# Kernel optimization log

Measured on AMD Instinct MI355X. Metric: run time of the kernel, lower is better.

Reference implementation:

```python
import jax, jax.numpy as jnp
import numpy as np

B, L, H, NH, P = 4, 1024, 1024, 16, 2048
HD = H // NH


def setup_inputs() -> dict:
    key = jax.random.key(0)
    ks = jax.random.split(key, 6)
    x = jax.random.normal(ks[0], (B, L, H), dtype=jnp.float32)
    # torch.nn.Linear weights are [out, in]
    Wqkv = jax.random.normal(ks[1], (3 * H, H), dtype=jnp.float32) * 0.02
    bqkv = jnp.zeros((3 * H,), dtype=jnp.float32)
    Wo = jax.random.normal(ks[2], (H, H), dtype=jnp.float32) * 0.02
    bo = jnp.zeros((H,), dtype=jnp.float32)
    Er = jax.random.normal(ks[3], (NH, P, HD), dtype=jnp.float32)
    # causal mask: True where attention is disallowed (masked_fill semantics)
    mask = jnp.triu(jnp.ones((L, L), dtype=bool), k=1)
    return {"x": x, "mask": mask, "Wqkv": Wqkv, "bqkv": bqkv,
            "Wo": Wo, "bo": bo, "Er": Er}


def reference(x, mask, Wqkv, bqkv, Wo, bo, Er):
    b, l, d = x.shape
    nh, p, hd = Er.shape
    qkv = x @ Wqkv.T + bqkv                      # [b, l, 3d]
    q, k, v = jnp.split(qkv, 3, axis=-1)
    q = q.reshape(b, l, nh, hd).transpose(0, 2, 1, 3)   # [b, nh, l, hd]
    k = k.reshape(b, l, nh, hd).transpose(0, 2, 1, 3)
    v = v.reshape(b, l, nh, hd).transpose(0, 2, 1, 3)

    scores = jnp.einsum('bnlh,bnkh->bnlk', q, k) / jnp.sqrt(
        jnp.asarray(hd, dtype=x.dtype))

    # relative positions (j - i), torch negative-index wraparound -> mod p
    pos = jnp.arange(l)
    rel = (pos[None, :] - pos[:, None]) % p      # [l, l] in [0, p)
    # Equivalent to einsum('bnlh,rnlkh->bnlk', q, Er[:, rel][None]) but
    # computed as q @ Er^T over all positions then gathered (same math,
    # avoids materializing the [nh, l, l, hd] tensor).
    QEr_full = jnp.einsum('bnlh,nph->bnlp', q, Er)       # [b, nh, l, p]
    i_idx = pos[:, None]                          # broadcasts with rel
    QEr = QEr_full[:, :, i_idx, rel]              # [b, nh, l, l]

    a = scores + QEr
    a = jnp.where(mask, -jnp.inf, a)
    a = jax.nn.softmax(a, axis=-1)                # dropout: eval mode (identity)

    out = jnp.einsum('bnlk,bnkh->bnlh', a, v)     # [b, nh, l, hd]
    out = out.transpose(0, 2, 1, 3).reshape(b, l, d)
    return out @ Wo.T + bo
```

## Files before the change

kernel.cpp:

```cpp
#include <hip/hip_runtime.h>

typedef unsigned short u16;
typedef __bf16 bf16x8 __attribute__((ext_vector_type(8)));
typedef unsigned short u16x8 __attribute__((ext_vector_type(8)));
typedef float f32x4 __attribute__((ext_vector_type(4)));

#define MFMA16(a, b, c) __builtin_amdgcn_mfma_f32_16x16x32_bf16((a), (b), (c), 0, 0, 0)

#define WAVE_LDS_FENCE() do { \
  asm volatile("s_waitcnt lgkmcnt(0)" ::: "memory"); \
  __builtin_amdgcn_sched_barrier(0); \
} while (0)

#define PHASE_BARRIER() do { \
  asm volatile("s_waitcnt vmcnt(0)" ::: "memory"); \
  __builtin_amdgcn_sched_barrier(0); \
  __builtin_amdgcn_s_barrier(); \
} while (0)

#define GLDS(gp, lp) __builtin_amdgcn_global_load_lds( \
    (const __attribute__((address_space(1))) unsigned int*)(gp), \
    (__attribute__((address_space(3))) unsigned int*)(lp), 16, 0, 0)

__device__ __forceinline__ u16 f2b(float f) {
  unsigned u = __float_as_uint(f);
  u += 0x7fffu + ((u >> 16) & 1u);
  return (u16)(u >> 16);
}
__device__ __forceinline__ float b2f(u16 h) {
  return __uint_as_float(((unsigned)h) << 16);
}

__global__ void cvt_all(const float* __restrict__ x, u16* __restrict__ xb,
                        const float* __restrict__ w1, u16* __restrict__ w1b,
                        const float* __restrict__ w2, u16* __restrict__ w2b) {
  int i = blockIdx.x * blockDim.x + threadIdx.x;
  const float* s; u16* d; int off;
  if (i < 1048576)      { s = x;  d = xb;  off = i; }
  else if (i < 1835008) { s = w1; d = w1b; off = i - 1048576; }
  else                  { s = w2; d = w2b; off = i - 1835008; }
  float4 v = *(const float4*)(s + (size_t)off * 4);
  *(ushort4*)(d + (size_t)off * 4) = make_ushort4(f2b(v.x), f2b(v.y), f2b(v.z), f2b(v.w));
}

__global__ void build_F(const float* __restrict__ Er, u16* __restrict__ Fb) {
  int i = blockIdx.x * blockDim.x + threadIdx.x;
  int base = i * 4;
  int d = base & 63;
  int m = (base >> 6) & 1023;
  int n = base >> 16;
  int sm = (2048 - m) & 2047;
  float4 v = *(const float4*)(Er + ((size_t)(n * 2048 + sm) * 64 + d));
  *(ushort4*)(Fb + (size_t)base) = make_ushort4(f2b(v.x), f2b(v.y), f2b(v.z), f2b(v.w));
}

__global__ __launch_bounds__(256) void transpose_v(const u16* __restrict__ V, u16* __restrict__ Vt) {
  __shared__ u16 T[4096];
  const int bn = blockIdx.x, i0 = blockIdx.y * 64;
  const int t = threadIdx.x;
#pragma unroll
  for (int s = 0; s < 2; ++s) {
    int ch = t + 256 * s;
    int i = ch >> 3, c = ch & 7;
    u16x8 v = *(const u16x8*)&V[(size_t)((bn << 10) + i0 + i) * 64 + c * 8];
#pragma unroll
    for (int e = 0; e < 8; ++e) {
      int d = c * 8 + e;
      T[d * 64 + ((((i >> 3) ^ (d & 7) ^ ((d >> 3) & 7)) & 7) << 3) + (i & 7)] = v[e];
    }
  }
  __syncthreads();
#pragma unroll
  for (int s = 0; s < 2; ++s) {
    int ch = t + 256 * s;
    int d = ch >> 3, cc = ch & 7;
    u16x8 o = *(const u16x8*)&T[d * 64 + (((cc ^ (d & 7) ^ ((d >> 3) & 7)) & 7) << 3)];
    *(u16x8*)&Vt[(size_t)((bn << 6) + d) * 1024 + i0 + cc * 8] = o;
  }
}

__global__ __launch_bounds__(256) void gemm_qkv(const u16* __restrict__ A, const u16* __restrict__ Bw,
                                                const float* __restrict__ bias,
                                                u16* __restrict__ Qo, u16* __restrict__ Ko,
                                                u16* __restrict__ Vo) {
  __shared__ u16 As[2][4][128][8];
  __shared__ u16 Bs[2][4][128][8];
  const int m0 = blockIdx.y * 128, n0 = blockIdx.x * 128;
  const int t = threadIdx.x, lane = t & 63, w = t >> 6;
  const int wr = w >> 1, wc = w & 1;
  const int l16 = lane & 15, lg = lane >> 4;
  f32x4 acc[4][4] = {};
  const int c0 = t, r0 = c0 & 127, g0 = c0 >> 7;
  const int c1 = t + 256, r1 = c1 & 127, g1 = c1 >> 7;

#define STAGE(buf, k0) do { \
    GLDS(&A[(size_t)(m0 + r0) * 1024 + (k0) + g0 * 8], &As[buf][g0][r0][0]); \
    GLDS(&A[(size_t)(m0 + r1) * 1024 + (k0) + g1 * 8], &As[buf][g1][r1][0]); \
    GLDS(&Bw[(size_t)(n0 + r0) * 1024 + (k0) + g0 * 8], &Bs[buf][g0][r0][0]); \
    GLDS(&Bw[(size_t)(n0 + r1) * 1024 + (k0) + g1 * 8], &Bs[buf][g1][r1][0]); \
  } while (0)

  STAGE(0, 0);
  PHASE_BARRIER();

#pragma unroll 2
  for (int kt = 0; kt < 32; ++kt) {
    const int buf = kt & 1;
    if (kt < 31) STAGE(buf ^ 1, (kt + 1) * 32);
    __builtin_amdgcn_sched_barrier(0);
    bf16x8 af[4], bfr[4];
#pragma unroll
    for (int m = 0; m < 4; ++m) af[m] = *(const bf16x8*)&As[buf][lg][wr * 64 + m * 16 + l16][0];
#pragma unroll
    for (int n = 0; n < 4; ++n) bfr[n] = *(const bf16x8*)&Bs[buf][lg][wc * 64 + n * 16 + l16][0];
#pragma unroll
    for (int m = 0; m < 4; ++m)
#pragma unroll
      for (int n = 0; n < 4; ++n) acc[m][n] = MFMA16(af[m], bfr[n], acc[m][n]);
    PHASE_BARRIER();
  }
#undef STAGE

#pragma unroll
  for (int n = 0; n < 4; ++n) {
    int col = n0 + wc * 64 + n * 16 + l16;
    float bq = bias[col];
    int which = col >> 10;
    int h = col & 1023;
    int head = h >> 6, d = h & 63;
    u16* dst = which == 0 ? Qo : (which == 1 ? Ko : Vo);
    float scale = which == 1 ? 0.125f : 1.0f;
#pragma unroll
    for (int m = 0; m < 4; ++m) {
#pragma unroll
      for (int r = 0; r < 4; ++r) {
        int row = m0 + wr * 64 + m * 16 + lg * 4 + r;
        int b = row >> 10, ii = row & 1023;
        float v = (acc[m][n][r] + bq) * scale;
        dst[(size_t)(((b * 16 + head) << 10) + ii) * 64 + d] = f2b(v);
      }
    }
  }
}

__global__ __launch_bounds__(256) void gemm_out(const u16* __restrict__ A, const u16* __restrict__ Bw,
                                                const float* __restrict__ bias, float* __restrict__ Co) {
  __shared__ u16 As[2][4][128][8];
  __shared__ u16 Bs[2][4][128][8];
  const int m0 = blockIdx.y * 128, n0 = blockIdx.x * 128;
  const int t = threadIdx.x, lane = t & 63, w = t >> 6;
  const int wr = w >> 1, wc = w & 1;
  const int l16 = lane & 15, lg = lane >> 4;
  f32x4 acc[4][4] = {};
  const int c0 = t, r0 = c0 & 127, g0 = c0 >> 7;
  const int c1 = t + 256, r1 = c1 & 127, g1 = c1 >> 7;

#define STAGE(buf, k0) do { \
    GLDS(&A[(size_t)(m0 + r0) * 1024 + (k0) + g0 * 8], &As[buf][g0][r0][0]); \
    GLDS(&A[(size_t)(m0 + r1) * 1024 + (k0) + g1 * 8], &As[buf][g1][r1][0]); \
    GLDS(&Bw[(size_t)(n0 + r0) * 1024 + (k0) + g0 * 8], &Bs[buf][g0][r0][0]); \
    GLDS(&Bw[(size_t)(n0 + r1) * 1024 + (k0) + g1 * 8], &Bs[buf][g1][r1][0]); \
  } while (0)

  STAGE(0, 0);
  PHASE_BARRIER();

#pragma unroll 2
  for (int kt = 0; kt < 32; ++kt) {
    const int buf = kt & 1;
    if (kt < 31) STAGE(buf ^ 1, (kt + 1) * 32);
    __builtin_amdgcn_sched_barrier(0);
    bf16x8 af[4], bfr[4];
#pragma unroll
    for (int m = 0; m < 4; ++m) af[m] = *(const bf16x8*)&As[buf][lg][wr * 64 + m * 16 + l16][0];
#pragma unroll
    for (int n = 0; n < 4; ++n) bfr[n] = *(const bf16x8*)&Bs[buf][lg][wc * 64 + n * 16 + l16][0];
#pragma unroll
    for (int m = 0; m < 4; ++m)
#pragma unroll
      for (int n = 0; n < 4; ++n) acc[m][n] = MFMA16(af[m], bfr[n], acc[m][n]);
    PHASE_BARRIER();
  }
#undef STAGE

#pragma unroll
  for (int n = 0; n < 4; ++n) {
    int col = n0 + wc * 64 + n * 16 + l16;
    float bq = bias[col];
#pragma unroll
    for (int m = 0; m < 4; ++m) {
#pragma unroll
      for (int r = 0; r < 4; ++r) {
        int row = m0 + wr * 64 + m * 16 + lg * 4 + r;
        Co[(size_t)row * 1024 + col] = acc[m][n][r] + bq;
      }
    }
  }
}

__global__ __launch_bounds__(256) void attn_kernel(const u16* __restrict__ Qg, const u16* __restrict__ Kg,
                                                   const u16* __restrict__ Vtg, const u16* __restrict__ Fg,
                                                   u16* __restrict__ AO) {
  __shared__ u16 Kl[4096];
  __shared__ u16 Vl[4096];
  __shared__ u16 Fl[8192];
  __shared__ u16 Bnd[4][16][84];
  __shared__ u16 Pl[4][1024];

  const int bn = blockIdx.x;
  const int b = bn >> 4, n = bn & 15;
  const int qt = 15 - (int)blockIdx.y;
  const int i0 = qt * 64;
  const int t = threadIdx.x, lane = t & 63, w = t >> 6;
  const int l16 = lane & 15, lg = lane >> 4;

  const int rr0 = t >> 3, cc0 = t & 7;
  const int rr1 = (t + 256) >> 3, cc1 = t & 7;
  const int rr2 = (t + 512) >> 3, cc2 = t & 7;
  const int rr3 = (t + 768) >> 3, cc3 = t & 7;

  bf16x8 qf[2];
  {
    const u16* qp = &Qg[(size_t)((bn << 10) + i0 + (w << 4) + l16) * 64 + lg * 8];
    qf[0] = *(const bf16x8*)qp;
    qf[1] = *(const bf16x8*)(qp + 32);
  }

  float mrun[4], lsum[4];
  f32x4 ao[4] = {};
#pragma unroll
  for (int r = 0; r < 4; ++r) { mrun[r] = -3.0e38f; lsum[r] = 0.0f; }

  u16x8 rk0, rk1, rv0, rv1, rf0, rf1, rf2, rf3;

#define LOAD_STAGE(jt_) do { \
    int j0_ = (jt_) * 64, mb_ = i0 - j0_ - 63; \
    rk0 = *(const u16x8*)&Kg[(size_t)((bn << 10) + j0_ + rr0) * 64 + cc0 * 8]; \
    rk1 = *(const u16x8*)&Kg[(size_t)((bn << 10) + j0_ + rr1) * 64 + cc1 * 8]; \
    rv0 = *(const u16x8*)&Vtg[(size_t)((bn << 6) + rr0) * 1024 + j0_ + cc0 * 8]; \
    rv1 = *(const u16x8*)&Vtg[(size_t)((bn << 6) + rr1) * 1024 + j0_ + cc1 * 8]; \
    int m0_ = mb_ + rr0; m0_ = m0_ < 0 ? 0 : (m0_ > 1023 ? 1023 : m0_); \
    int m1_ = mb_ + rr1; m1_ = m1_ < 0 ? 0 : (m1_ > 1023 ? 1023 : m1_); \
    int m2_ = mb_ + rr2; m2_ = m2_ < 0 ? 0 : (m2_ > 1023 ? 1023 : m2_); \
    int m3_ = mb_ + rr3; m3_ = m3_ < 0 ? 0 : (m3_ > 1023 ? 1023 : m3_); \
    rf0 = *(const u16x8*)&Fg[(size_t)((n << 10) + m0_) * 64 + cc0 * 8]; \
    rf1 = *(const u16x8*)&Fg[(size_t)((n << 10) + m1_) * 64 + cc1 * 8]; \
    rf2 = *(const u16x8*)&Fg[(size_t)((n << 10) + m2_) * 64 + cc2 * 8]; \
    rf3 = *(const u16x8*)&Fg[(size_t)((n << 10) + m3_) * 64 + cc3 * 8]; \
  } while (0)

  LOAD_STAGE(0);

  for (int jt = 0; jt <= qt; ++jt) {
    const bool diag = (jt == qt);

    *(u16x8*)&Kl[rr0 * 64 + (((cc0 ^ (rr0 & 7)) & 7) << 3)] = rk0;
    *(u16x8*)&Kl[rr1 * 64 + (((cc1 ^ (rr1 & 7)) & 7) << 3)] = rk1;
    *(u16x8*)&Vl[rr0 * 64 + (((cc0 ^ (rr0 & 7)) & 7) << 3)] = rv0;
    *(u16x8*)&Vl[rr1 * 64 + (((cc1 ^ (rr1 & 7)) & 7) << 3)] = rv1;
    *(u16x8*)&Fl[rr0 * 64 + (((cc0 ^ (rr0 & 7)) & 7) << 3)] = rf0;
    *(u16x8*)&Fl[rr1 * 64 + (((cc1 ^ (rr1 & 7)) & 7) << 3)] = rf1;
    *(u16x8*)&Fl[rr2 * 64 + (((cc2 ^ (rr2 & 7)) & 7) << 3)] = rf2;
    *(u16x8*)&Fl[rr3 * 64 + (((cc3 ^ (rr3 & 7)) & 7) << 3)] = rf3;
    __syncthreads();

    if (jt < qt) LOAD_STAGE(jt + 1);

    f32x4 sc[4] = {};
#pragma unroll
    for (int kk = 0; kk < 2; ++kk)
#pragma unroll
      for (int nn = 0; nn < 4; ++nn) {
        int jr = nn * 16 + l16;
        bf16x8 kb = *(const bf16x8*)&Kl[jr * 64 + ((((lg + 4 * kk) ^ (jr & 7)) & 7) << 3)];
        sc[nn] = MFMA16(qf[kk], kb, sc[nn]);
      }
    f32x4 bb[5] = {};
#pragma unroll
    for (int kk = 0; kk < 2; ++kk)
#pragma unroll
      for (int ct = 0; ct < 5; ++ct) {
        int trow = (w << 4) + ct * 16 + l16;
        bf16x8 fb = *(const bf16x8*)&Fl[trow * 64 + ((((lg + 4 * kk) ^ (trow & 7)) & 7) << 3)];
        bb[ct] = MFMA16(qf[kk], fb, bb[ct]);
      }
#pragma unroll
    for (int ct = 0; ct < 5; ++ct)
#pragma unroll
      for (int r = 0; r < 4; ++r)
        Bnd[w][lg * 4 + r][ct * 16 + l16] = f2b(bb[ct][r]);
    WAVE_LDS_FENCE();

    const unsigned* bw = (const unsigned*)&Bnd[w][0][0];
    float pv[4][4];
#pragma unroll
    for (int r = 0; r < 4; ++r) {
      int il = lg * 4 + r;
      int c0 = il - l16 + 63;
      int u0 = il * 84 + c0;
      int sh = (u0 & 1) << 4;
      float stmp[4];
      float mx = -3.0e38f;
#pragma unroll
      for (int nn = 0; nn < 4; ++nn) {
        unsigned dv = bw[(u0 >> 1) - 8 * nn];
        float s = sc[nn][r] + b2f((u16)((dv >> sh) & 0xffffu));
        if (diag && (c0 - 16 * nn + (w << 4) < 63)) s = -1.0e30f;
        stmp[nn] = s;
        mx = fmaxf(mx, s);
      }
#pragma unroll
      for (int off = 1; off < 16; off <<= 1) mx = fmaxf(mx, __shfl_xor(mx, off));
      float mnew = fmaxf(mrun[r], mx);
      float scl = __expf(mrun[r] - mnew);
      float rs = 0.0f;
#pragma unroll
      for (int nn = 0; nn < 4; ++nn) {
        pv[nn][r] = __expf(stmp[nn] - mnew);
        rs += pv[nn][r];
      }
      lsum[r] = lsum[r] * scl + rs;
      mrun[r] = mnew;
#pragma unroll
      for (int nd = 0; nd < 4; ++nd) ao[nd][r] *= scl;
    }

#pragma unroll
    for (int nn = 0; nn < 4; ++nn)
#pragma unroll
      for (int r = 0; r < 4; ++r) {
        int i = lg * 4 + r, j = nn * 16 + l16;
        Pl[w][i * 64 + ((((j >> 3) ^ (i & 7)) & 7) << 3) + (j & 7)] = f2b(pv[nn][r]);
      }
    WAVE_LDS_FENCE();
#pragma unroll
    for (int kk = 0; kk < 2; ++kk) {
      bf16x8 pa = *(const bf16x8*)&Pl[w][l16 * 64 + ((((lg + 4 * kk) ^ (l16 & 7)) & 7) << 3)];
#pragma unroll
      for (int nd = 0; nd < 4; ++nd) {
        int dr = nd * 16 + l16;
        bf16x8 vb = *(const bf16x8*)&Vl[dr * 64 + ((((lg + 4 * kk) ^ (dr & 7)) & 7) << 3)];
        ao[nd] = MFMA16(pa, vb, ao[nd]);
      }
    }
    __syncthreads();
  }

#pragma unroll
  for (int r = 0; r < 4; ++r)
#pragma unroll
    for (int off = 1; off < 16; off <<= 1) lsum[r] += __shfl_xor(lsum[r], off);

#pragma unroll
  for (int nd = 0; nd < 4; ++nd)
#pragma unroll
    for (int r = 0; r < 4; ++r) {
      int i = i0 + (w << 4) + lg * 4 + r;
      int d = nd * 16 + l16;
      float v = ao[nd][r] / lsum[r];
      AO[(size_t)((b << 10) + i) * 1024 + n * 64 + d] = f2b(v);
    }
#undef LOAD_STAGE
}

extern "C" void kernel_launch(void* const* d_in, const int* in_sizes, int n_in,
                              void* d_out, int out_size, void* d_ws, size_t ws_size,
                              hipStream_t stream) {
  (void)in_sizes; (void)n_in; (void)out_size; (void)ws_size;
  const float* x    = (const float*)d_in[0];
  const float* Wqkv = (const float*)d_in[2];
  const float* bqkv = (const float*)d_in[3];
  const float* Wo   = (const float*)d_in[4];
  const float* bo   = (const float*)d_in[5];
  const float* Er   = (const float*)d_in[6];
  float* out = (float*)d_out;

  char* p = (char*)d_ws;
  u16* xb    = (u16*)p; p += (size_t)4096 * 1024 * 2;
  u16* wqkvb = (u16*)p; p += (size_t)3072 * 1024 * 2;
  u16* wob   = (u16*)p; p += (size_t)1024 * 1024 * 2;
  u16* Fb    = (u16*)p; p += (size_t)16 * 1024 * 64 * 2;
  u16* Qb    = (u16*)p; p += (size_t)64 * 1024 * 64 * 2;
  u16* Kb    = (u16*)p; p += (size_t)64 * 1024 * 64 * 2;
  u16* Vb    = (u16*)p; p += (size_t)64 * 1024 * 64 * 2;
  u16* Vtb   = (u16*)p; p += (size_t)64 * 1024 * 64 * 2;
  u16* AO    = (u16*)p; p += (size_t)4096 * 1024 * 2;

  cvt_all<<<8192, 256, 0, stream>>>(x, xb, Wqkv, wqkvb, Wo, wob);
  build_F<<<1024, 256, 0, stream>>>(Er, Fb);
  gemm_qkv<<<dim3(24, 32), 256, 0, stream>>>(xb, wqkvb, bqkv, Qb, Kb, Vb);
  transpose_v<<<dim3(64, 16), 256, 0, stream>>>(Vb, Vtb);
  attn_kernel<<<dim3(64, 16), 256, 0, stream>>>(Qb, Kb, Vtb, Fb, AO);
  gemm_out<<<dim3(8, 32), 256, 0, stream>>>(AO, wob, bo, out);
}
```

Baseline: 166.2 us.

## Triple-buffer GEMM pipelines, remap tiles per XCD, and reuse Er band rows in attention

Both GEMMs move from double-buffered LDS staging with a full vmcnt(0) wait to a three-stage ring that waits on vmcnt(4), so one prefetch stays in flight behind each compute step. Block indices are remapped so consecutive tiles on the same XCD share A/B rows, aiming at better L2 reuse. In attention, the relative-position Er band is kept in a two-half ring in LDS, so each step loads only 64 new rows instead of 128. The band gather is rewritten into a compact per-wave layout read as one u16x4 vector. s_setprio is raised around the MFMA sections. The changes add LDS use and index arithmetic, and depend on correct wait counts and ring indexing.

Result: faster. 153.0 us (-7.9%).

```diff
diff --git a/kernel.cpp b/kernel.cpp
--- a/kernel.cpp
+++ b/kernel.cpp
@@ -3,6 +3,7 @@
 typedef unsigned short u16;
 typedef __bf16 bf16x8 __attribute__((ext_vector_type(8)));
 typedef unsigned short u16x8 __attribute__((ext_vector_type(8)));
+typedef unsigned short u16x4 __attribute__((ext_vector_type(4)));
 typedef float f32x4 __attribute__((ext_vector_type(4)));
 
 #define MFMA16(a, b, c) __builtin_amdgcn_mfma_f32_16x16x32_bf16((a), (b), (c), 0, 0, 0)
@@ -12,10 +13,11 @@
   __builtin_amdgcn_sched_barrier(0); \
 } while (0)
 
-#define PHASE_BARRIER() do { \
-  asm volatile("s_waitcnt vmcnt(0)" ::: "memory"); \
+#define PIPE_WAIT(N) do { \
+  asm volatile("s_waitcnt vmcnt(" #N ")" ::: "memory"); \
   __builtin_amdgcn_sched_barrier(0); \
   __builtin_amdgcn_s_barrier(); \
+  __builtin_amdgcn_sched_barrier(0); \
 } while (0)
 
 #define GLDS(gp, lp) __builtin_amdgcn_global_load_lds( \
@@ -83,31 +85,38 @@
                                                 const float* __restrict__ bias,
                                                 u16* __restrict__ Qo, u16* __restrict__ Ko,
                                                 u16* __restrict__ Vo) {
-  __shared__ u16 As[2][4][128][8];
-  __shared__ u16 Bs[2][4][128][8];
-  const int m0 = blockIdx.y * 128, n0 = blockIdx.x * 128;
+  __shared__ u16 As[3][4][128][8];
+  __shared__ u16 Bs[3][4][128][8];
+  const int orig = blockIdx.y * 24 + blockIdx.x;
+  const int xcd = orig & 7, q = orig >> 3;
+  const int mt = ((xcd >> 1) << 3) + q / 12;
+  const int nt = (xcd & 1) * 12 + q % 12;
+  const int m0 = mt * 128, n0 = nt * 128;
   const int t = threadIdx.x, lane = t & 63, w = t >> 6;
   const int wr = w >> 1, wc = w & 1;
   const int l16 = lane & 15, lg = lane >> 4;
   f32x4 acc[4][4] = {};
-  const int c0 = t, r0 = c0 & 127, g0 = c0 >> 7;
-  const int c1 = t + 256, r1 = c1 & 127, g1 = c1 >> 7;
+  const int r0 = t & 127, g0 = t >> 7;
+  const int g1 = g0 + 2;
 
 #define STAGE(buf, k0) do { \
     GLDS(&A[(size_t)(m0 + r0) * 1024 + (k0) + g0 * 8], &As[buf][g0][r0][0]); \
-    GLDS(&A[(size_t)(m0 + r1) * 1024 + (k0) + g1 * 8], &As[buf][g1][r1][0]); \
+    GLDS(&A[(size_t)(m0 + r0) * 1024 + (k0) + g1 * 8], &As[buf][g1][r0][0]); \
     GLDS(&Bw[(size_t)(n0 + r0) * 1024 + (k0) + g0 * 8], &Bs[buf][g0][r0][0]); \
-    GLDS(&Bw[(size_t)(n0 + r1) * 1024 + (k0) + g1 * 8], &Bs[buf][g1][r1][0]); \
+    GLDS(&Bw[(size_t)(n0 + r0) * 1024 + (k0) + g1 * 8], &Bs[buf][g1][r0][0]); \
   } while (0)
 
   STAGE(0, 0);
-  PHASE_BARRIER();
-
-#pragma unroll 2
+  STAGE(1, 32);
+
+  int buf = 0;
   for (int kt = 0; kt < 32; ++kt) {
-    const int buf = kt & 1;
-    if (kt < 31) STAGE(buf ^ 1, (kt + 1) * 32);
-    __builtin_amdgcn_sched_barrier(0);
+    if (kt < 31) PIPE_WAIT(4); else PIPE_WAIT(0);
+    if (kt < 30) {
+      int nb = buf + 2; if (nb >= 3) nb -= 3;
+      STAGE(nb, (kt + 2) * 32);
+      __builtin_amdgcn_sched_barrier(0);
+    }
     bf16x8 af[4], bfr[4];
 #pragma unroll
     for (int m = 0; m < 4; ++m) af[m] = *(const bf16x8*)&As[buf][lg][wr * 64 + m * 16 + l16][0];
@@ -117,7 +126,7 @@
     for (int m = 0; m < 4; ++m)
 #pragma unroll
       for (int n = 0; n < 4; ++n) acc[m][n] = MFMA16(af[m], bfr[n], acc[m][n]);
-    PHASE_BARRIER();
+    if (++buf == 3) buf = 0;
   }
 #undef STAGE
 
@@ -145,31 +154,38 @@
 
 __global__ __launch_bounds__(256) void gemm_out(const u16* __restrict__ A, const u16* __restrict__ Bw,
                                                 const float* __restrict__ bias, float* __restrict__ Co) {
-  __shared__ u16 As[2][4][128][8];
-  __shared__ u16 Bs[2][4][128][8];
-  const int m0 = blockIdx.y * 128, n0 = blockIdx.x * 128;
+  __shared__ u16 As[3][4][128][8];
+  __shared__ u16 Bs[3][4][128][8];
+  const int orig = blockIdx.y * 8 + blockIdx.x;
+  const int xcd = orig & 7, q = orig >> 3;
+  const int mt = (xcd << 2) + (q >> 3);
+  const int nt = q & 7;
+  const int m0 = mt * 128, n0 = nt * 128;
   const int t = threadIdx.x, lane = t & 63, w = t >> 6;
   const int wr = w >> 1, wc = w & 1;
   const int l16 = lane & 15, lg = lane >> 4;
   f32x4 acc[4][4] = {};
-  const int c0 = t, r0 = c0 & 127, g0 = c0 >> 7;
-  const int c1 = t + 256, r1 = c1 & 127, g1 = c1 >> 7;
+  const int r0 = t & 127, g0 = t >> 7;
+  const int g1 = g0 + 2;
 
 #define STAGE(buf, k0) do { \
     GLDS(&A[(size_t)(m0 + r0) * 1024 + (k0) + g0 * 8], &As[buf][g0][r0][0]); \
-    GLDS(&A[(size_t)(m0 + r1) * 1024 + (k0) + g1 * 8], &As[buf][g1][r1][0]); \
+    GLDS(&A[(size_t)(m0 + r0) * 1024 + (k0) + g1 * 8], &As[buf][g1][r0][0]); \
     GLDS(&Bw[(size_t)(n0 + r0) * 1024 + (k0) + g0 * 8], &Bs[buf][g0][r0][0]); \
-    GLDS(&Bw[(size_t)(n0 + r1) * 1024 + (k0) + g1 * 8], &Bs[buf][g1][r1][0]); \
+    GLDS(&Bw[(size_t)(n0 + r0) * 1024 + (k0) + g1 * 8], &Bs[buf][g1][r0][0]); \
   } while (0)
 
   STAGE(0, 0);
-  PHASE_BARRIER();
-
-#pragma unroll 2
+  STAGE(1, 32);
+
+  int buf = 0;
   for (int kt = 0; kt < 32; ++kt) {
-    const int buf = kt & 1;
-    if (kt < 31) STAGE(buf ^ 1, (kt + 1) * 32);
-    __builtin_amdgcn_sched_barrier(0);
+    if (kt < 31) PIPE_WAIT(4); else PIPE_WAIT(0);
+    if (kt < 30) {
+      int nb = buf + 2; if (nb >= 3) nb -= 3;
+      STAGE(nb, (kt + 2) * 32);
+      __builtin_amdgcn_sched_barrier(0);
+    }
     bf16x8 af[4], bfr[4];
 #pragma unroll
     for (int m = 0; m < 4; ++m) af[m] = *(const bf16x8*)&As[buf][lg][wr * 64 + m * 16 + l16][0];
@@ -179,7 +195,7 @@
     for (int m = 0; m < 4; ++m)
 #pragma unroll
       for (int n = 0; n < 4; ++n) acc[m][n] = MFMA16(af[m], bfr[n], acc[m][n]);
-    PHASE_BARRIER();
+    if (++buf == 3) buf = 0;
   }
 #undef STAGE
 
@@ -204,7 +220,7 @@
   __shared__ u16 Kl[4096];
   __shared__ u16 Vl[4096];
   __shared__ u16 Fl[8192];
-  __shared__ u16 Bnd[4][16][84];
+  __shared__ u16 Bnd2[4][1024];
   __shared__ u16 Pl[4][1024];
 
   const int bn = blockIdx.x;
@@ -216,8 +232,6 @@
 
   const int rr0 = t >> 3, cc0 = t & 7;
   const int rr1 = (t + 256) >> 3, cc1 = t & 7;
-  const int rr2 = (t + 512) >> 3, cc2 = t & 7;
-  const int rr3 = (t + 768) >> 3, cc3 = t & 7;
 
   bf16x8 qf[2];
   {
@@ -226,12 +240,23 @@
     qf[1] = *(const bf16x8*)(qp + 32);
   }
 
+  {
+    int mb0 = i0 - 63;
+    int h0 = 64 + rr0, h1 = 64 + rr1;
+    int gm0 = mb0 + h0; gm0 = gm0 < 0 ? 0 : (gm0 > 1023 ? 1023 : gm0);
+    int gm1 = mb0 + h1; gm1 = gm1 < 0 ? 0 : (gm1 > 1023 ? 1023 : gm1);
+    u16x8 a = *(const u16x8*)&Fg[(size_t)((n << 10) + gm0) * 64 + cc0 * 8];
+    u16x8 c = *(const u16x8*)&Fg[(size_t)((n << 10) + gm1) * 64 + cc1 * 8];
+    *(u16x8*)&Fl[h0 * 64 + (((cc0 ^ (h0 & 7)) & 7) << 3)] = a;
+    *(u16x8*)&Fl[h1 * 64 + (((cc1 ^ (h1 & 7)) & 7) << 3)] = c;
+  }
+
   float mrun[4], lsum[4];
   f32x4 ao[4] = {};
 #pragma unroll
   for (int r = 0; r < 4; ++r) { mrun[r] = -3.0e38f; lsum[r] = 0.0f; }
 
-  u16x8 rk0, rk1, rv0, rv1, rf0, rf1, rf2, rf3;
+  u16x8 rk0, rk1, rv0, rv1, rf0, rf1;
 
 #define LOAD_STAGE(jt_) do { \
     int j0_ = (jt_) * 64, mb_ = i0 - j0_ - 63; \
@@ -241,31 +266,27 @@
     rv1 = *(const u16x8*)&Vtg[(size_t)((bn << 6) + rr1) * 1024 + j0_ + cc1 * 8]; \
     int m0_ = mb_ + rr0; m0_ = m0_ < 0 ? 0 : (m0_ > 1023 ? 1023 : m0_); \
     int m1_ = mb_ + rr1; m1_ = m1_ < 0 ? 0 : (m1_ > 1023 ? 1023 : m1_); \
-    int m2_ = mb_ + rr2; m2_ = m2_ < 0 ? 0 : (m2_ > 1023 ? 1023 : m2_); \
-    int m3_ = mb_ + rr3; m3_ = m3_ < 0 ? 0 : (m3_ > 1023 ? 1023 : m3_); \
     rf0 = *(const u16x8*)&Fg[(size_t)((n << 10) + m0_) * 64 + cc0 * 8]; \
     rf1 = *(const u16x8*)&Fg[(size_t)((n << 10) + m1_) * 64 + cc1 * 8]; \
-    rf2 = *(const u16x8*)&Fg[(size_t)((n << 10) + m2_) * 64 + cc2 * 8]; \
-    rf3 = *(const u16x8*)&Fg[(size_t)((n << 10) + m3_) * 64 + cc3 * 8]; \
   } while (0)
 
   LOAD_STAGE(0);
 
   for (int jt = 0; jt <= qt; ++jt) {
     const bool diag = (jt == qt);
+    const int ph = (jt & 1) << 6;
 
     *(u16x8*)&Kl[rr0 * 64 + (((cc0 ^ (rr0 & 7)) & 7) << 3)] = rk0;
     *(u16x8*)&Kl[rr1 * 64 + (((cc1 ^ (rr1 & 7)) & 7) << 3)] = rk1;
     *(u16x8*)&Vl[rr0 * 64 + (((cc0 ^ (rr0 & 7)) & 7) << 3)] = rv0;
     *(u16x8*)&Vl[rr1 * 64 + (((cc1 ^ (rr1 & 7)) & 7) << 3)] = rv1;
-    *(u16x8*)&Fl[rr0 * 64 + (((cc0 ^ (rr0 & 7)) & 7) << 3)] = rf0;
-    *(u16x8*)&Fl[rr1 * 64 + (((cc1 ^ (rr1 & 7)) & 7) << 3)] = rf1;
-    *(u16x8*)&Fl[rr2 * 64 + (((cc2 ^ (rr2 & 7)) & 7) << 3)] = rf2;
-    *(u16x8*)&Fl[rr3 * 64 + (((cc3 ^ (rr3 & 7)) & 7) << 3)] = rf3;
+    *(u16x8*)&Fl[(rr0 ^ ph) * 64 + (((cc0 ^ (rr0 & 7)) & 7) << 3)] = rf0;
+    *(u16x8*)&Fl[(rr1 ^ ph) * 64 + (((cc1 ^ (rr1 & 7)) & 7) << 3)] = rf1;
     __syncthreads();
 
     if (jt < qt) LOAD_STAGE(jt + 1);
 
+    __builtin_amdgcn_s_setprio(1);
     f32x4 sc[4] = {};
 #pragma unroll
     for (int kk = 0; kk < 2; ++kk)
@@ -281,31 +302,34 @@
 #pragma unroll
       for (int ct = 0; ct < 5; ++ct) {
         int trow = (w << 4) + ct * 16 + l16;
-        bf16x8 fb = *(const bf16x8*)&Fl[trow * 64 + ((((lg + 4 * kk) ^ (trow & 7)) & 7) << 3)];
+        bf16x8 fb = *(const bf16x8*)&Fl[(trow ^ ph) * 64 + ((((lg + 4 * kk) ^ (trow & 7)) & 7) << 3)];
         bb[ct] = MFMA16(qf[kk], fb, bb[ct]);
       }
+    __builtin_amdgcn_s_setprio(0);
+
 #pragma unroll
     for (int ct = 0; ct < 5; ++ct)
 #pragma unroll
-      for (int r = 0; r < 4; ++r)
-        Bnd[w][lg * 4 + r][ct * 16 + l16] = f2b(bb[ct][r]);
+      for (int r = 0; r < 4; ++r) {
+        int il = lg * 4 + r;
+        int jl = il + 63 - (ct * 16 + l16);
+        if ((unsigned)jl < 64u)
+          Bnd2[w][il * 64 + ((jl & 15) << 2) + (jl >> 4)] = f2b(bb[ct][r]);
+      }
     WAVE_LDS_FENCE();
 
-    const unsigned* bw = (const unsigned*)&Bnd[w][0][0];
     float pv[4][4];
 #pragma unroll
     for (int r = 0; r < 4; ++r) {
       int il = lg * 4 + r;
-      int c0 = il - l16 + 63;
-      int u0 = il * 84 + c0;
-      int sh = (u0 & 1) << 4;
+      u16x4 gv = *(const u16x4*)&Bnd2[w][il * 64 + (l16 << 2)];
       float stmp[4];
       float mx = -3.0e38f;
 #pragma unroll
       for (int nn = 0; nn < 4; ++nn) {
-        unsigned dv = bw[(u0 >> 1) - 8 * nn];
-        float s = sc[nn][r] + b2f((u16)((dv >> sh) & 0xffffu));
-        if (diag && (c0 - 16 * nn + (w << 4) < 63)) s = -1.0e30f;
+        int jl = nn * 16 + l16;
+        float s = sc[nn][r] + b2f(gv[nn]);
+        if (diag && jl > (w << 4) + il) s = -1.0e30f;
         stmp[nn] = s;
         mx = fmaxf(mx, s);
       }
@@ -333,6 +357,7 @@
         Pl[w][i * 64 + ((((j >> 3) ^ (i & 7)) & 7) << 3) + (j & 7)] = f2b(pv[nn][r]);
       }
     WAVE_LDS_FENCE();
+    __builtin_amdgcn_s_setprio(1);
 #pragma unroll
     for (int kk = 0; kk < 2; ++kk) {
       bf16x8 pa = *(const bf16x8*)&Pl[w][l16 * 64 + ((((lg + 4 * kk) ^ (l16 & 7)) & 7) << 3)];
@@ -343,6 +368,7 @@
         ao[nd] = MFMA16(pa, vb, ao[nd]);
       }
     }
+    __builtin_amdgcn_s_setprio(0);
     __syncthreads();
   }
 
```
